# Kernel tuning notes

Measured on AMD Instinct MI355X. Metric: run time of the kernel, lower is better.

The kernel has to match this reference:

```python
import jax, jax.numpy as jnp
import numpy as np

V = 50000
E = 300000
B = 4
LAT = 512
H = 128
L = 3


def setup_inputs() -> dict:
    key = jax.random.key(0)
    ks = jax.random.split(key, 8)
    vertex_xyz = jax.random.normal(ks[0], (V, 3), jnp.float32)
    latent = jax.random.normal(ks[1], (B, LAT), jnp.float32)
    edge_index = jax.random.randint(ks[2], (2, E), 0, V, dtype=jnp.int32)
    def lin(k, out_f, in_f):
        return jax.random.normal(k, (out_f, in_f), jnp.float32) / np.float32(np.sqrt(in_f))
    W_in = lin(ks[3], H, LAT + 3)
    b_in = jnp.zeros((H,), jnp.float32)
    conv_W = jax.random.normal(ks[4], (L, H, H), jnp.float32) / np.float32(np.sqrt(H))
    conv_b = jnp.zeros((L, H), jnp.float32)
    W_out = lin(ks[5], 3, H)
    b_out = jnp.zeros((3,), jnp.float32)
    return dict(vertex_xyz=vertex_xyz, latent=latent, edge_index=edge_index,
                W_in=W_in, b_in=b_in, conv_W=conv_W, conv_b=conv_b,
                W_out=W_out, b_out=b_out)


def _edge_norm(edge_index, B_, V_):
    """GCN symmetric normalization for edge_index tiled B times (same node ids,
    as in the original code's edge_index.repeat(1, B)) plus self-loops on all
    N = B*V flattened nodes. Structure is identical across layers, so compute once."""
    N = B_ * V_
    ei = jnp.tile(edge_index, (1, B_))                 # (2, E*B), ids in [0, V)
    loops = jnp.arange(N, dtype=edge_index.dtype)
    row = jnp.concatenate([ei[0], loops])              # source
    col = jnp.concatenate([ei[1], loops])              # target
    deg = jax.ops.segment_sum(jnp.ones(row.shape, jnp.float32), col, num_segments=N)
    dis = jnp.where(deg > 0, jax.lax.rsqrt(jnp.maximum(deg, 1.0)), 0.0)
    norm = dis[row] * dis[col]                         # (E*B + N,)
    return row, col, norm, N


def reference(vertex_xyz, latent, edge_index, W_in, b_in, conv_W, conv_b, W_out, b_out):
    B_, V_ = latent.shape[0], vertex_xyz.shape[0]
    row, col, norm, N = _edge_norm(edge_index, B_, V_)

    # concat template xyz with broadcast latent -> (B*V, LAT+3)
    x = jnp.concatenate([
        jnp.broadcast_to(vertex_xyz[None], (B_, V_, 3)),
        jnp.broadcast_to(latent[:, None, :], (B_, V_, latent.shape[-1])),
    ], axis=-1).reshape(B_ * V_, -1)

    x = jax.nn.relu(x @ W_in.T + b_in)                 # (N, H)

    for l in range(conv_W.shape[0]):
        h = x @ conv_W[l].T                            # linear (no bias before aggregation)
        agg = jax.ops.segment_sum(norm[:, None] * h[row], col, num_segments=N)
        x = jax.nn.relu(agg + conv_b[l])

    out = x @ W_out.T + b_out                          # (N, 3)
    return out.reshape(B_, V_, 3)
```

## Files before the change

kernel.cpp:

```cpp
#include <hip/hip_runtime.h>
#include <hip/hip_bf16.h>

typedef __attribute__((ext_vector_type(8))) short short8;
typedef __attribute__((ext_vector_type(4))) float f32x4;

#define V_ 50000
#define E_ 300000
#define B_ 4
#define LAT_ 512
#define H_ 128
#define L_ 3
#define N_ (B_*V_)

#define SCAN_B 512
#define SCAN_G ((V_ + SCAN_B - 1) / SCAN_B)

__device__ inline void bsplit(float v, ushort& hi, ushort& lo) {
    __hip_bfloat16 hb = __float2bfloat16(v);
    float hf = __bfloat162float(hb);
    __hip_bfloat16 lb = __float2bfloat16(v - hf);
    hi = *(ushort*)&hb; lo = *(ushort*)&lb;
}
__device__ inline float bjoin(ushort h, ushort l) {
    __hip_bfloat16 hb = *(__hip_bfloat16*)&h;
    __hip_bfloat16 lb = *(__hip_bfloat16*)&l;
    return __bfloat162float(hb) + __bfloat162float(lb);
}
__device__ inline int swzr(int row) { return ((row & 7) << 4) ^ ((row & 8) << 2); }


__global__ void k_zero(int* __restrict__ deg, int* __restrict__ cursor) {
    int i = blockIdx.x * 256 + threadIdx.x;
    if (i < V_) { deg[i] = 0; cursor[i] = 0; }
}

__global__ void k_deg(const int* __restrict__ dst, int* __restrict__ deg) {
    int e = blockIdx.x * 256 + threadIdx.x;
    if (e < E_) atomicAdd(&deg[dst[e]], 1);
}

__global__ __launch_bounds__(SCAN_B) void k_scan1(const int* __restrict__ deg,
                                                  int* __restrict__ off,
                                                  float* __restrict__ dis,
                                                  int* __restrict__ part) {
    int t = threadIdx.x;
    int i = blockIdx.x * SCAN_B + t;
    int d = (i < V_) ? deg[i] : 0;
    __shared__ int sm[SCAN_B];
    sm[t] = d;
    __syncthreads();
    int val = d;
    for (int s = 1; s < SCAN_B; s <<= 1) {
        int o = (t >= s) ? sm[t - s] : 0;
        __syncthreads();
        val += o;
        sm[t] = val;
        __syncthreads();
    }
    if (i < V_) {
        off[i] = val - d;
        dis[i] = rsqrtf((float)(B_ * d + 1));
    }
    if (t == SCAN_B - 1) part[blockIdx.x] = val;
}

__global__ void k_scan2(int* __restrict__ part) {
    __shared__ int sm[128];
    int t = threadIdx.x;
    int v = (t < SCAN_G) ? part[t] : 0;
    sm[t] = v;
    __syncthreads();
    int val = v;
    for (int s = 1; s < 128; s <<= 1) {
        int o = (t >= s) ? sm[t - s] : 0;
        __syncthreads();
        val += o;
        sm[t] = val;
        __syncthreads();
    }
    if (t < SCAN_G) part[t] = val - v;
}

__global__ __launch_bounds__(SCAN_B) void k_scan3(int* __restrict__ off,
                                                  const int* __restrict__ part) {
    int i = blockIdx.x * SCAN_B + threadIdx.x;
    if (i < V_) off[i] += part[blockIdx.x];
    if (i == 0) off[V_] = E_;
}

__global__ void k_fill(const int* __restrict__ src, const int* __restrict__ dst,
                       const int* __restrict__ off, int* __restrict__ cursor,
                       int* __restrict__ csr) {
    int e = blockIdx.x * 256 + threadIdx.x;
    if (e < E_) {
        int c = dst[e];
        int p = atomicAdd(&cursor[c], 1);
        csr[off[c] + p] = src[e];
    }
}


__global__ void k_wsplit(const float* __restrict__ W, ushort* __restrict__ Whi,
                         ushort* __restrict__ Wlo) {
    int i = blockIdx.x * 256 + threadIdx.x;
    float w = W[i];
    ushort hi, lo; bsplit(w, hi, lo);
    Whi[i] = hi; Wlo[i] = lo;
}

__global__ void k_prep(const float* __restrict__ Win, float* __restrict__ Wxyz) {
    int j = threadIdx.x;
    f32x4 v = {Win[(size_t)j*(LAT_+3)+0], Win[(size_t)j*(LAT_+3)+1],
               Win[(size_t)j*(LAT_+3)+2], 0.f};
    *(f32x4*)(Wxyz + j*4) = v;
}

__global__ void k_latproj(const float* __restrict__ Win, const float* __restrict__ bin,
                          const float* __restrict__ latent, float* __restrict__ latproj) {
    int t = blockIdx.x * 128 + threadIdx.x;
    if (t >= B_ * H_) return;
    int b = t >> 7, j = t & 127;
    const float* wr = Win + (size_t)j * (LAT_ + 3) + 3;
    const float* lp = latent + (size_t)b * LAT_;
    float s = bin[j];
    for (int k = 0; k < LAT_; k++) s = fmaf(wr[k], lp[k], s);
    latproj[t] = s;
}


__global__ __launch_bounds__(512, 2) void k_big(
        const float* __restrict__ xyz, const float* __restrict__ latproj,
        const float* __restrict__ Wxyz,
        const ushort* __restrict__ Whi, const ushort* __restrict__ Wlo,
        const float* __restrict__ convb,
        const float* __restrict__ Wout, const float* __restrict__ bout,
        float* __restrict__ out) {
    __shared__ __align__(16) char smem[32768];
    const int tid = threadIdx.x;
    const int row0 = V_ + blockIdx.x * 64;
    const int lane = tid & 63;
    const int wid  = tid >> 6;
    const int l15  = lane & 15;
    const int kg   = lane >> 4;
    const int n0   = wid * 16;
    const int tr   = tid >> 4;
    const int c0   = (tid & 15) * 8;

#pragma unroll
    for (int rep = 0; rep < 2; rep++) {
        int row = tr + rep * 32;
        int node = row0 + row;
        ushort hs[8], ls[8];
        if (node < N_) {
            int v = node % V_, b = node / V_;
            float xv0 = xyz[v*3+0], xv1 = xyz[v*3+1], xv2 = xyz[v*3+2];
#pragma unroll
            for (int i = 0; i < 8; i++) {
                int j = c0 + i;
                f32x4 wx = *(const f32x4*)(Wxyz + j*4);
                float s = latproj[b*H_ + j];
                s = fmaf(wx[0], xv0, s);
                s = fmaf(wx[1], xv1, s);
                s = fmaf(wx[2], xv2, s);
                s = fmaxf(s, 0.f);
                bsplit(s, hs[i], ls[i]);
            }
        } else {
#pragma unroll
            for (int i = 0; i < 8; i++) { hs[i] = 0; ls[i] = 0; }
        }
        int bo = (c0*2) ^ swzr(row);
        *(uint4*)(smem + row*256 + bo) = *(uint4*)hs;
        *(uint4*)(smem + 16384 + row*256 + bo) = *(uint4*)ls;
    }
    __syncthreads();

    for (int l = 0; l < L_; l++) {
        const ushort* Whp = Whi + (size_t)l*H_*H_;
        const ushort* Wlp = Wlo + (size_t)l*H_*H_;
        short8 wh[4], wl[4];
#pragma unroll
        for (int ks = 0; ks < 4; ks++) {
            const ushort* bh = Whp + (size_t)(n0 + l15)*H_ + ks*32 + kg*4;
            const ushort* bl = Wlp + (size_t)(n0 + l15)*H_ + ks*32 + kg*4;
            union { short8 v; uint2 u[2]; } uh, ul;
            uh.u[0] = *(const uint2*)bh;  uh.u[1] = *(const uint2*)(bh + 16);
            ul.u[0] = *(const uint2*)bl;  ul.u[1] = *(const uint2*)(bl + 16);
            wh[ks] = uh.v; wl[ks] = ul.v;
        }
        f32x4 acc[4];
#pragma unroll
        for (int mt = 0; mt < 4; mt++) acc[mt] = (f32x4){0.f,0.f,0.f,0.f};
#pragma unroll
        for (int mt = 0; mt < 4; mt++) {
            int row = mt*16 + l15;
            int sw = swzr(row);
            const char* rbh = smem + row*256;
            const char* rbl = smem + 16384 + row*256;
#pragma unroll
            for (int ks = 0; ks < 4; ks++) {
                int cc = ks*64 + kg*8;
                union { short8 v; uint2 u[2]; } ah, al;
                ah.u[0] = *(const uint2*)(rbh + (cc ^ sw));
                ah.u[1] = *(const uint2*)(rbh + ((cc+32) ^ sw));
                al.u[0] = *(const uint2*)(rbl + (cc ^ sw));
                al.u[1] = *(const uint2*)(rbl + ((cc+32) ^ sw));
                acc[mt] = __builtin_amdgcn_mfma_f32_16x16x32_bf16(ah.v, wh[ks], acc[mt], 0,0,0);
                acc[mt] = __builtin_amdgcn_mfma_f32_16x16x32_bf16(al.v, wh[ks], acc[mt], 0,0,0);
                acc[mt] = __builtin_amdgcn_mfma_f32_16x16x32_bf16(ah.v, wl[ks], acc[mt], 0,0,0);
            }
        }
        __syncthreads();
        float bv = convb[l*H_ + n0 + l15];
        int bo = (n0 + l15) * 2;
#pragma unroll
        for (int mt = 0; mt < 4; mt++)
#pragma unroll
            for (int j = 0; j < 4; j++) {
                int row = mt*16 + kg*4 + j;
                int sw = swzr(row);
                float v = fmaxf(acc[mt][j] + bv, 0.f);
                ushort hi, lo; bsplit(v, hi, lo);
                *(ushort*)(smem + row*256 + (bo ^ sw)) = hi;
                *(ushort*)(smem + 16384 + row*256 + (bo ^ sw)) = lo;
            }
        __syncthreads();
    }

    float wo0[8], wo1[8], wo2[8];
#pragma unroll
    for (int i = 0; i < 8; i++) {
        wo0[i] = Wout[0*H_ + c0 + i];
        wo1[i] = Wout[1*H_ + c0 + i];
        wo2[i] = Wout[2*H_ + c0 + i];
    }
#pragma unroll
    for (int rep = 0; rep < 2; rep++) {
        int row = tr + rep*32;
        int node = row0 + row;
        int bo = (c0*2) ^ swzr(row);
        uint4 uh = *(const uint4*)(smem + row*256 + bo);
        uint4 ul = *(const uint4*)(smem + 16384 + row*256 + bo);
        const ushort* hp = (const ushort*)&uh;
        const ushort* lp = (const ushort*)&ul;
        float p0 = 0.f, p1 = 0.f, p2 = 0.f;
#pragma unroll
        for (int i = 0; i < 8; i++) {
            float xv = bjoin(hp[i], lp[i]);
            p0 = fmaf(xv, wo0[i], p0);
            p1 = fmaf(xv, wo1[i], p1);
            p2 = fmaf(xv, wo2[i], p2);
        }
#pragma unroll
        for (int m = 1; m < 16; m <<= 1) {
            p0 += __shfl_xor(p0, m);
            p1 += __shfl_xor(p1, m);
            p2 += __shfl_xor(p2, m);
        }
        if ((tid & 15) == 0 && node < N_) {
            out[(size_t)node*3 + 0] = p0 + bout[0];
            out[(size_t)node*3 + 1] = p1 + bout[1];
            out[(size_t)node*3 + 2] = p2 + bout[2];
        }
    }
}


template<int MODE>
__global__ __launch_bounds__(512, 2) void k_lay0(
        const ushort* __restrict__ xh, const ushort* __restrict__ xl,
        const float* __restrict__ xyz, const float* __restrict__ latproj,
        const float* __restrict__ Wxyz,
        const ushort* __restrict__ Whp, const ushort* __restrict__ Wlp,
        float* __restrict__ h) {
    __shared__ __align__(16) char smem[32768];
    const int tid = threadIdx.x;
    const int row0 = blockIdx.x * 64;
    const int lane = tid & 63;
    const int wid  = tid >> 6;
    const int l15  = lane & 15;
    const int kg   = lane >> 4;
    const int n0   = wid * 16;
    const int tr   = tid >> 4;
    const int c0   = (tid & 15) * 8;

    if (MODE == 0) {
#pragma unroll
        for (int rep = 0; rep < 2; rep++) {
            int row = tr + rep * 32;
            int v = row0 + row;
            ushort hs[8], ls[8];
            if (v < V_) {
                float xv0 = xyz[v*3+0], xv1 = xyz[v*3+1], xv2 = xyz[v*3+2];
#pragma unroll
                for (int i = 0; i < 8; i++) {
                    int j = c0 + i;
                    f32x4 wx = *(const f32x4*)(Wxyz + j*4);
                    float s = latproj[j];
                    s = fmaf(wx[0], xv0, s);
                    s = fmaf(wx[1], xv1, s);
                    s = fmaf(wx[2], xv2, s);
                    s = fmaxf(s, 0.f);
                    bsplit(s, hs[i], ls[i]);
                }
            } else {
#pragma unroll
                for (int i = 0; i < 8; i++) { hs[i] = 0; ls[i] = 0; }
            }
            int bo = (c0*2) ^ swzr(row);
            *(uint4*)(smem + row*256 + bo) = *(uint4*)hs;
            *(uint4*)(smem + 16384 + row*256 + bo) = *(uint4*)ls;
        }
    } else {
#pragma unroll
        for (int k = 0; k < 4; k++) {
            int chunk = tid + k*512;
            int p  = chunk >> 10;
            int r  = (chunk >> 4) & 63;
            int cb = (chunk & 15) * 16;
            int grow = row0 + r;
            uint4 g = {0u,0u,0u,0u};
            if (grow < V_)
                g = *(const uint4*)((const char*)((p ? xl : xh) + (size_t)grow*H_) + cb);
            *(uint4*)(smem + p*16384 + r*256 + (cb ^ swzr(r))) = g;
        }
    }
    __syncthreads();

    short8 wh[4], wl[4];
#pragma unroll
    for (int ks = 0; ks < 4; ks++) {
        const ushort* bh = Whp + (size_t)(n0 + l15)*H_ + ks*32 + kg*4;
        const ushort* bl = Wlp + (size_t)(n0 + l15)*H_ + ks*32 + kg*4;
        union { short8 v; uint2 u[2]; } uh, ul;
        uh.u[0] = *(const uint2*)bh;  uh.u[1] = *(const uint2*)(bh + 16);
        ul.u[0] = *(const uint2*)bl;  ul.u[1] = *(const uint2*)(bl + 16);
        wh[ks] = uh.v; wl[ks] = ul.v;
    }

    f32x4 acc[4];
#pragma unroll
    for (int mt = 0; mt < 4; mt++) acc[mt] = (f32x4){0.f,0.f,0.f,0.f};
#pragma unroll
    for (int mt = 0; mt < 4; mt++) {
        int row = mt*16 + l15;
        int sw = swzr(row);
        const char* rbh = smem + row*256;
        const char* rbl = smem + 16384 + row*256;
#pragma unroll
        for (int ks = 0; ks < 4; ks++) {
            int cc = ks*64 + kg*8;
            union { short8 v; uint2 u[2]; } ah, al;
            ah.u[0] = *(const uint2*)(rbh + (cc ^ sw));
            ah.u[1] = *(const uint2*)(rbh + ((cc+32) ^ sw));
            al.u[0] = *(const uint2*)(rbl + (cc ^ sw));
            al.u[1] = *(const uint2*)(rbl + ((cc+32) ^ sw));
            acc[mt] = __builtin_amdgcn_mfma_f32_16x16x32_bf16(ah.v, wh[ks], acc[mt], 0,0,0);
            acc[mt] = __builtin_amdgcn_mfma_f32_16x16x32_bf16(al.v, wh[ks], acc[mt], 0,0,0);
            acc[mt] = __builtin_amdgcn_mfma_f32_16x16x32_bf16(ah.v, wl[ks], acc[mt], 0,0,0);
        }
    }

#pragma unroll
    for (int mt = 0; mt < 4; mt++)
#pragma unroll
        for (int j = 0; j < 4; j++) {
            int grow = row0 + mt*16 + kg*4 + j;
            if (grow < V_) h[(size_t)grow*H_ + n0 + l15] = acc[mt][j];
        }
}


template<bool FINAL>
__global__ __launch_bounds__(256) void k_agg0(const float* __restrict__ h,
                                              const float* __restrict__ dis,
                                              const int* __restrict__ off,
                                              const int* __restrict__ csr,
                                              const float* __restrict__ bias,
                                              ushort* __restrict__ xh_out,
                                              ushort* __restrict__ xl_out,
                                              const float* __restrict__ Wout,
                                              const float* __restrict__ bout,
                                              float* __restrict__ out) {
    int c = blockIdx.x * 4 + (threadIdx.x >> 6);
    int lane = threadIdx.x & 63;
    if (c >= V_) return;
    int beg = off[c], end = off[c + 1];
    int nu = end - beg;
    int   myu  = (lane < nu) ? csr[beg + lane] : 0;
    float mywu = (lane < nu) ? dis[myu] : 0.f;
    float a0 = 0.f, a1 = 0.f;
    int nn = nu < 64 ? nu : 64;
    for (int i = 0; i < nn; i++) {
        int u = __shfl(myu, i);
        float wu = __shfl(mywu, i);
        const float* hu = h + (size_t)u * 128;
        a0 = fmaf(wu, hu[lane],      a0);
        a1 = fmaf(wu, hu[lane + 64], a1);
    }
    for (int i = beg + 64; i < end; i++) {
        int u = csr[i];
        float wu = dis[u];
        const float* hu = h + (size_t)u * 128;
        a0 = fmaf(wu, hu[lane],      a0);
        a1 = fmaf(wu, hu[lane + 64], a1);
    }
    float dc = dis[c];
    const float* hr = h + (size_t)c * 128;
    float s0 = fmaxf(dc * (float)B_ * a0 + dc * dc * hr[lane]      + bias[lane],      0.f);
    float s1 = fmaxf(dc * (float)B_ * a1 + dc * dc * hr[lane + 64] + bias[lane + 64], 0.f);
    if (FINAL) {
        float p0 = s0 * Wout[0*H_ + lane] + s1 * Wout[0*H_ + 64 + lane];
        float p1 = s0 * Wout[1*H_ + lane] + s1 * Wout[1*H_ + 64 + lane];
        float p2 = s0 * Wout[2*H_ + lane] + s1 * Wout[2*H_ + 64 + lane];
#pragma unroll
        for (int d = 32; d; d >>= 1) {
            p0 += __shfl_down(p0, d);
            p1 += __shfl_down(p1, d);
            p2 += __shfl_down(p2, d);
        }
        if (lane == 0) {
            out[(size_t)c*3 + 0] = p0 + bout[0];
            out[(size_t)c*3 + 1] = p1 + bout[1];
            out[(size_t)c*3 + 2] = p2 + bout[2];
        }
    } else {
        ushort h0, l0, h1, l1;
        bsplit(s0, h0, l0);
        bsplit(s1, h1, l1);
        xh_out[(size_t)c*128 + lane]      = h0;
        xl_out[(size_t)c*128 + lane]      = l0;
        xh_out[(size_t)c*128 + lane + 64] = h1;
        xl_out[(size_t)c*128 + lane + 64] = l1;
    }
}


extern "C" void kernel_launch(void* const* d_in, const int* in_sizes, int n_in,
                              void* d_out, int out_size, void* d_ws, size_t ws_size,
                              hipStream_t stream) {
    const float* xyz    = (const float*)d_in[0];
    const float* latent = (const float*)d_in[1];
    const int*   ei     = (const int*)d_in[2];
    const float* Win    = (const float*)d_in[3];
    const float* bin    = (const float*)d_in[4];
    const float* convW  = (const float*)d_in[5];
    const float* convb  = (const float*)d_in[6];
    const float* Wout   = (const float*)d_in[7];
    const float* bout   = (const float*)d_in[8];
    float* out = (float*)d_out;

    char* w = (char*)d_ws;
    auto carve = [&](size_t bytes) {
        char* p = w;
        w += (bytes + 255) & ~(size_t)255;
        return p;
    };
    ushort* xh      = (ushort*)carve((size_t)V_ * H_ * 2);
    ushort* xl      = (ushort*)carve((size_t)V_ * H_ * 2);
    float*  h       = (float*)carve((size_t)V_ * H_ * 4);
    ushort* Whi     = (ushort*)carve((size_t)L_ * H_ * H_ * 2);
    ushort* Wlo     = (ushort*)carve((size_t)L_ * H_ * H_ * 2);
    float*  dis     = (float*)carve((size_t)V_ * 4);
    float*  latproj = (float*)carve((size_t)B_ * H_ * 4);
    float*  Wxyz    = (float*)carve((size_t)H_ * 4 * 4);
    int*    deg     = (int*)carve((size_t)V_ * 4);
    int*    off     = (int*)carve((size_t)(V_ + 1) * 4);
    int*    cursor  = (int*)carve((size_t)V_ * 4);
    int*    csr     = (int*)carve((size_t)E_ * 4);
    int*    part    = (int*)carve((size_t)SCAN_G * 4);
    (void)ws_size; (void)in_sizes; (void)n_in; (void)out_size;

    const int* src = ei;
    const int* dst = ei + E_;

    k_zero<<<(V_ + 255) / 256, 256, 0, stream>>>(deg, cursor);
    k_deg<<<(E_ + 255) / 256, 256, 0, stream>>>(dst, deg);
    k_scan1<<<SCAN_G, SCAN_B, 0, stream>>>(deg, off, dis, part);
    k_scan2<<<1, 128, 0, stream>>>(part);
    k_scan3<<<SCAN_G, SCAN_B, 0, stream>>>(off, part);
    k_fill<<<(E_ + 255) / 256, 256, 0, stream>>>(src, dst, off, cursor, csr);

    k_wsplit<<<(L_ * H_ * H_) / 256, 256, 0, stream>>>(convW, Whi, Wlo);
    k_prep<<<1, 128, 0, stream>>>(Win, Wxyz);
    k_latproj<<<4, 128, 0, stream>>>(Win, bin, latent, latproj);

    k_big<<<(N_ - V_ + 63) / 64, 512, 0, stream>>>(xyz, latproj, Wxyz, Whi, Wlo,
                                                   convb, Wout, bout, out);

    const int GB0 = (V_ + 63) / 64;
    k_lay0<0><<<GB0, 512, 0, stream>>>(nullptr, nullptr, xyz, latproj, Wxyz,
                                       Whi, Wlo, h);
    k_agg0<false><<<(V_ + 3) / 4, 256, 0, stream>>>(h, dis, off, csr, convb,
                                                    xh, xl, nullptr, nullptr, nullptr);
    k_lay0<1><<<GB0, 512, 0, stream>>>(xh, xl, nullptr, nullptr, nullptr,
                                       Whi + (size_t)1*H_*H_, Wlo + (size_t)1*H_*H_, h);
    k_agg0<false><<<(V_ + 3) / 4, 256, 0, stream>>>(h, dis, off, csr, convb + 1*H_,
                                                    xh, xl, nullptr, nullptr, nullptr);
    k_lay0<1><<<GB0, 512, 0, stream>>>(xh, xl, nullptr, nullptr, nullptr,
                                       Whi + (size_t)2*H_*H_, Wlo + (size_t)2*H_*H_, h);
    k_agg0<true><<<(V_ + 3) / 4, 256, 0, stream>>>(h, dis, off, csr, convb + 2*H_,
                                                   nullptr, nullptr, Wout, bout, out);
}
```

Baseline: 416.1 us.

## Keep GEMM activations in registers, stream weights as A-operand, drop LDS round-trips

Restructures the dense MLP kernels so each wave owns 32 nodes and holds their activations as MFMA B-fragments in registers. Weight tiles are streamed as the A operand, and layer outputs are converted straight back into B-fragments without going through shared memory or block barriers. This removes the LDS staging, the swizzled stores and the __syncthreads between layers in k_big and k_lay0, and lets k_lay0 write vectorised f32x4 outputs. In exchange every wave reloads all of W from global/L2 for each layer, and register pressure rises with the 16 accumulators plus fragments.

```diff
diff --git a/kernel.cpp b/kernel.cpp
--- a/kernel.cpp
+++ b/kernel.cpp
@@ -21,12 +21,6 @@
     __hip_bfloat16 lb = __float2bfloat16(v - hf);
     hi = *(ushort*)&hb; lo = *(ushort*)&lb;
 }
-__device__ inline float bjoin(ushort h, ushort l) {
-    __hip_bfloat16 hb = *(__hip_bfloat16*)&h;
-    __hip_bfloat16 lb = *(__hip_bfloat16*)&l;
-    return __bfloat162float(hb) + __bfloat162float(lb);
-}
-__device__ inline int swzr(int row) { return ((row & 7) << 4) ^ ((row & 8) << 2); }
 
 
 __global__ void k_zero(int* __restrict__ deg, int* __restrict__ cursor) {
@@ -128,246 +122,219 @@
 }
 
 
-__global__ __launch_bounds__(512, 2) void k_big(
+__device__ inline void gemm_layer(const ushort* __restrict__ Ah,
+                                  const ushort* __restrict__ Al,
+                                  int l15, int kg,
+                                  const short8 bh[4][2], const short8 bl[4][2],
+                                  f32x4 acc[8][2]) {
+#pragma unroll
+    for (int m = 0; m < 8; m++) {
+        const ushort* ph = Ah + (m*16 + l15)*H_ + kg*4;
+        const ushort* pl = Al + (m*16 + l15)*H_ + kg*4;
+        short8 ah[4], al[4];
+#pragma unroll
+        for (int ks = 0; ks < 4; ks++) {
+            union { short8 v; uint2 u[2]; } uh, ul;
+            uh.u[0] = *(const uint2*)(ph + ks*32);
+            uh.u[1] = *(const uint2*)(ph + ks*32 + 16);
+            ul.u[0] = *(const uint2*)(pl + ks*32);
+            ul.u[1] = *(const uint2*)(pl + ks*32 + 16);
+            ah[ks] = uh.v; al[ks] = ul.v;
+        }
+#pragma unroll
+        for (int ks = 0; ks < 4; ks++)
+#pragma unroll
+            for (int nt = 0; nt < 2; nt++) {
+                acc[m][nt] = __builtin_amdgcn_mfma_f32_16x16x32_bf16(ah[ks], bh[ks][nt], acc[m][nt], 0,0,0);
+                acc[m][nt] = __builtin_amdgcn_mfma_f32_16x16x32_bf16(ah[ks], bl[ks][nt], acc[m][nt], 0,0,0);
+                acc[m][nt] = __builtin_amdgcn_mfma_f32_16x16x32_bf16(al[ks], bh[ks][nt], acc[m][nt], 0,0,0);
+            }
+    }
+}
+
+__device__ inline void acc_to_bfrag(const f32x4 acc[8][2], const float* __restrict__ bias,
+                                    int kg, short8 bh[4][2], short8 bl[4][2]) {
+#pragma unroll
+    for (int t = 0; t < 4; t++)
+#pragma unroll
+        for (int nt = 0; nt < 2; nt++) {
+            union { short8 v; ushort s[8]; } uh, ul;
+#pragma unroll
+            for (int q = 0; q < 2; q++) {
+                int m = 2*t + q;
+                f32x4 b4 = *(const f32x4*)(bias + m*16 + kg*4);
+#pragma unroll
+                for (int j = 0; j < 4; j++) {
+                    float s = fmaxf(acc[m][nt][j] + b4[j], 0.f);
+                    bsplit(s, uh.s[q*4+j], ul.s[q*4+j]);
+                }
+            }
+            bh[t][nt] = uh.v; bl[t][nt] = ul.v;
+        }
+}
+
+__device__ inline void x0_bfrag(const float* __restrict__ xyz, const float* __restrict__ lp,
+                                const float* __restrict__ Wxyz, int v, bool ok, int kg, int nt,
+                                short8 bh[4][2], short8 bl[4][2]) {
+    float x0 = xyz[v*3+0], x1 = xyz[v*3+1], x2 = xyz[v*3+2];
+#pragma unroll
+    for (int ks = 0; ks < 4; ks++) {
+        union { short8 v; ushort s[8]; } uh, ul;
+#pragma unroll
+        for (int q = 0; q < 2; q++)
+#pragma unroll
+            for (int j = 0; j < 4; j++) {
+                int f = ks*32 + q*16 + kg*4 + j;
+                f32x4 wx = *(const f32x4*)(Wxyz + f*4);
+                float s = lp[f];
+                s = fmaf(wx[0], x0, s);
+                s = fmaf(wx[1], x1, s);
+                s = fmaf(wx[2], x2, s);
+                s = fmaxf(s, 0.f);
+                if (!ok) s = 0.f;
+                bsplit(s, uh.s[q*4+j], ul.s[q*4+j]);
+            }
+        bh[ks][nt] = uh.v; bl[ks][nt] = ul.v;
+    }
+}
+
+
+__global__ __launch_bounds__(256, 2) void k_big2(
         const float* __restrict__ xyz, const float* __restrict__ latproj,
         const float* __restrict__ Wxyz,
         const ushort* __restrict__ Whi, const ushort* __restrict__ Wlo,
         const float* __restrict__ convb,
         const float* __restrict__ Wout, const float* __restrict__ bout,
         float* __restrict__ out) {
-    __shared__ __align__(16) char smem[32768];
-    const int tid = threadIdx.x;
-    const int row0 = V_ + blockIdx.x * 64;
+    const int tid  = threadIdx.x;
     const int lane = tid & 63;
-    const int wid  = tid >> 6;
     const int l15  = lane & 15;
     const int kg   = lane >> 4;
-    const int n0   = wid * 16;
-    const int tr   = tid >> 4;
-    const int c0   = (tid & 15) * 8;
-
-#pragma unroll
-    for (int rep = 0; rep < 2; rep++) {
-        int row = tr + rep * 32;
-        int node = row0 + row;
-        ushort hs[8], ls[8];
-        if (node < N_) {
-            int v = node % V_, b = node / V_;
-            float xv0 = xyz[v*3+0], xv1 = xyz[v*3+1], xv2 = xyz[v*3+2];
-#pragma unroll
-            for (int i = 0; i < 8; i++) {
-                int j = c0 + i;
-                f32x4 wx = *(const f32x4*)(Wxyz + j*4);
-                float s = latproj[b*H_ + j];
-                s = fmaf(wx[0], xv0, s);
-                s = fmaf(wx[1], xv1, s);
-                s = fmaf(wx[2], xv2, s);
-                s = fmaxf(s, 0.f);
-                bsplit(s, hs[i], ls[i]);
-            }
-        } else {
-#pragma unroll
-            for (int i = 0; i < 8; i++) { hs[i] = 0; ls[i] = 0; }
-        }
-        int bo = (c0*2) ^ swzr(row);
-        *(uint4*)(smem + row*256 + bo) = *(uint4*)hs;
-        *(uint4*)(smem + 16384 + row*256 + bo) = *(uint4*)ls;
-    }
-    __syncthreads();
-
+    const int base = V_ + (blockIdx.x * 4 + (tid >> 6)) * 32;
+
+    int node[2], vv[2]; bool ok[2];
+    const float* lp[2];
+#pragma unroll
+    for (int nt = 0; nt < 2; nt++) {
+        int n = base + nt*16 + l15;
+        ok[nt] = (n < N_);
+        int nn = ok[nt] ? n : 0;
+        node[nt] = nn;
+        int b = nn / V_;
+        vv[nt] = nn - b * V_;
+        lp[nt] = latproj + b * H_;
+    }
+
+    short8 bh[4][2], bl[4][2];
+#pragma unroll
+    for (int nt = 0; nt < 2; nt++)
+        x0_bfrag(xyz, lp[nt], Wxyz, vv[nt], ok[nt], kg, nt, bh, bl);
+
+    f32x4 acc[8][2];
     for (int l = 0; l < L_; l++) {
-        const ushort* Whp = Whi + (size_t)l*H_*H_;
-        const ushort* Wlp = Wlo + (size_t)l*H_*H_;
-        short8 wh[4], wl[4];
-#pragma unroll
-        for (int ks = 0; ks < 4; ks++) {
-            const ushort* bh = Whp + (size_t)(n0 + l15)*H_ + ks*32 + kg*4;
-            const ushort* bl = Wlp + (size_t)(n0 + l15)*H_ + ks*32 + kg*4;
-            union { short8 v; uint2 u[2]; } uh, ul;
-            uh.u[0] = *(const uint2*)bh;  uh.u[1] = *(const uint2*)(bh + 16);
-            ul.u[0] = *(const uint2*)bl;  ul.u[1] = *(const uint2*)(bl + 16);
-            wh[ks] = uh.v; wl[ks] = ul.v;
-        }
-        f32x4 acc[4];
-#pragma unroll
-        for (int mt = 0; mt < 4; mt++) acc[mt] = (f32x4){0.f,0.f,0.f,0.f};
-#pragma unroll
-        for (int mt = 0; mt < 4; mt++) {
-            int row = mt*16 + l15;
-            int sw = swzr(row);
-            const char* rbh = smem + row*256;
-            const char* rbl = smem + 16384 + row*256;
-#pragma unroll
-            for (int ks = 0; ks < 4; ks++) {
-                int cc = ks*64 + kg*8;
-                union { short8 v; uint2 u[2]; } ah, al;
-                ah.u[0] = *(const uint2*)(rbh + (cc ^ sw));
-                ah.u[1] = *(const uint2*)(rbh + ((cc+32) ^ sw));
-                al.u[0] = *(const uint2*)(rbl + (cc ^ sw));
-                al.u[1] = *(const uint2*)(rbl + ((cc+32) ^ sw));
-                acc[mt] = __builtin_amdgcn_mfma_f32_16x16x32_bf16(ah.v, wh[ks], acc[mt], 0,0,0);
-                acc[mt] = __builtin_amdgcn_mfma_f32_16x16x32_bf16(al.v, wh[ks], acc[mt], 0,0,0);
-                acc[mt] = __builtin_amdgcn_mfma_f32_16x16x32_bf16(ah.v, wl[ks], acc[mt], 0,0,0);
-            }
-        }
-        __syncthreads();
-        float bv = convb[l*H_ + n0 + l15];
-        int bo = (n0 + l15) * 2;
-#pragma unroll
-        for (int mt = 0; mt < 4; mt++)
+#pragma unroll
+        for (int m = 0; m < 8; m++)
+#pragma unroll
+            for (int nt = 0; nt < 2; nt++) acc[m][nt] = (f32x4){0.f,0.f,0.f,0.f};
+        gemm_layer(Whi + (size_t)l*H_*H_, Wlo + (size_t)l*H_*H_, l15, kg, bh, bl, acc);
+        if (l < L_ - 1)
+            acc_to_bfrag(acc, convb + l*H_, kg, bh, bl);
+    }
+
+    float p[2][3];
+#pragma unroll
+    for (int nt = 0; nt < 2; nt++) { p[nt][0] = 0.f; p[nt][1] = 0.f; p[nt][2] = 0.f; }
+#pragma unroll
+    for (int m = 0; m < 8; m++) {
+        f32x4 b4 = *(const f32x4*)(convb + 2*H_ + m*16 + kg*4);
+        f32x4 w0 = *(const f32x4*)(Wout + 0*H_ + m*16 + kg*4);
+        f32x4 w1 = *(const f32x4*)(Wout + 1*H_ + m*16 + kg*4);
+        f32x4 w2 = *(const f32x4*)(Wout + 2*H_ + m*16 + kg*4);
+#pragma unroll
+        for (int nt = 0; nt < 2; nt++)
 #pragma unroll
             for (int j = 0; j < 4; j++) {
-                int row = mt*16 + kg*4 + j;
-                int sw = swzr(row);
-                float v = fmaxf(acc[mt][j] + bv, 0.f);
-                ushort hi, lo; bsplit(v, hi, lo);
-                *(ushort*)(smem + row*256 + (bo ^ sw)) = hi;
-                *(ushort*)(smem + 16384 + row*256 + (bo ^ sw)) = lo;
-            }
-        __syncthreads();
-    }
-
-    float wo0[8], wo1[8], wo2[8];
-#pragma unroll
-    for (int i = 0; i < 8; i++) {
-        wo0[i] = Wout[0*H_ + c0 + i];
-        wo1[i] = Wout[1*H_ + c0 + i];
-        wo2[i] = Wout[2*H_ + c0 + i];
-    }
-#pragma unroll
-    for (int rep = 0; rep < 2; rep++) {
-        int row = tr + rep*32;
-        int node = row0 + row;
-        int bo = (c0*2) ^ swzr(row);
-        uint4 uh = *(const uint4*)(smem + row*256 + bo);
-        uint4 ul = *(const uint4*)(smem + 16384 + row*256 + bo);
-        const ushort* hp = (const ushort*)&uh;
-        const ushort* lp = (const ushort*)&ul;
-        float p0 = 0.f, p1 = 0.f, p2 = 0.f;
-#pragma unroll
-        for (int i = 0; i < 8; i++) {
-            float xv = bjoin(hp[i], lp[i]);
-            p0 = fmaf(xv, wo0[i], p0);
-            p1 = fmaf(xv, wo1[i], p1);
-            p2 = fmaf(xv, wo2[i], p2);
-        }
-#pragma unroll
-        for (int m = 1; m < 16; m <<= 1) {
-            p0 += __shfl_xor(p0, m);
-            p1 += __shfl_xor(p1, m);
-            p2 += __shfl_xor(p2, m);
-        }
-        if ((tid & 15) == 0 && node < N_) {
-            out[(size_t)node*3 + 0] = p0 + bout[0];
-            out[(size_t)node*3 + 1] = p1 + bout[1];
-            out[(size_t)node*3 + 2] = p2 + bout[2];
-        }
+                float s = fmaxf(acc[m][nt][j] + b4[j], 0.f);
+                p[nt][0] = fmaf(s, w0[j], p[nt][0]);
+                p[nt][1] = fmaf(s, w1[j], p[nt][1]);
+                p[nt][2] = fmaf(s, w2[j], p[nt][2]);
+            }
+    }
+#pragma unroll
+    for (int nt = 0; nt < 2; nt++)
+#pragma unroll
+        for (int o = 0; o < 3; o++) {
+            p[nt][o] += __shfl_xor(p[nt][o], 16);
+            p[nt][o] += __shfl_xor(p[nt][o], 32);
+        }
+    if (kg == 0) {
+#pragma unroll
+        for (int nt = 0; nt < 2; nt++)
+            if (ok[nt]) {
+                out[(size_t)node[nt]*3 + 0] = p[nt][0] + bout[0];
+                out[(size_t)node[nt]*3 + 1] = p[nt][1] + bout[1];
+                out[(size_t)node[nt]*3 + 2] = p[nt][2] + bout[2];
+            }
     }
 }
 
 
 template<int MODE>
-__global__ __launch_bounds__(512, 2) void k_lay0(
+__global__ __launch_bounds__(256, 2) void k_lay0(
         const ushort* __restrict__ xh, const ushort* __restrict__ xl,
         const float* __restrict__ xyz, const float* __restrict__ latproj,
         const float* __restrict__ Wxyz,
         const ushort* __restrict__ Whp, const ushort* __restrict__ Wlp,
         float* __restrict__ h) {
-    __shared__ __align__(16) char smem[32768];
-    const int tid = threadIdx.x;
-    const int row0 = blockIdx.x * 64;
+    const int tid  = threadIdx.x;
     const int lane = tid & 63;
-    const int wid  = tid >> 6;
     const int l15  = lane & 15;
     const int kg   = lane >> 4;
-    const int n0   = wid * 16;
-    const int tr   = tid >> 4;
-    const int c0   = (tid & 15) * 8;
-
+    const int base = (blockIdx.x * 4 + (tid >> 6)) * 32;
+
+    int node[2]; bool ok[2];
+#pragma unroll
+    for (int nt = 0; nt < 2; nt++) {
+        int n = base + nt*16 + l15;
+        ok[nt] = (n < V_);
+        node[nt] = ok[nt] ? n : 0;
+    }
+
+    short8 bh[4][2], bl[4][2];
     if (MODE == 0) {
 #pragma unroll
-        for (int rep = 0; rep < 2; rep++) {
-            int row = tr + rep * 32;
-            int v = row0 + row;
-            ushort hs[8], ls[8];
-            if (v < V_) {
-                float xv0 = xyz[v*3+0], xv1 = xyz[v*3+1], xv2 = xyz[v*3+2];
-#pragma unroll
-                for (int i = 0; i < 8; i++) {
-                    int j = c0 + i;
-                    f32x4 wx = *(const f32x4*)(Wxyz + j*4);
-                    float s = latproj[j];
-                    s = fmaf(wx[0], xv0, s);
-                    s = fmaf(wx[1], xv1, s);
-                    s = fmaf(wx[2], xv2, s);
-                    s = fmaxf(s, 0.f);
-                    bsplit(s, hs[i], ls[i]);
-                }
-            } else {
-#pragma unroll
-                for (int i = 0; i < 8; i++) { hs[i] = 0; ls[i] = 0; }
-            }
-            int bo = (c0*2) ^ swzr(row);
-            *(uint4*)(smem + row*256 + bo) = *(uint4*)hs;
-            *(uint4*)(smem + 16384 + row*256 + bo) = *(uint4*)ls;
-        }
+        for (int nt = 0; nt < 2; nt++)
+            x0_bfrag(xyz, latproj, Wxyz, node[nt], ok[nt], kg, nt, bh, bl);
     } else {
 #pragma unroll
-        for (int k = 0; k < 4; k++) {
-            int chunk = tid + k*512;
-            int p  = chunk >> 10;
-            int r  = (chunk >> 4) & 63;
-            int cb = (chunk & 15) * 16;
-            int grow = row0 + r;
-            uint4 g = {0u,0u,0u,0u};
-            if (grow < V_)
-                g = *(const uint4*)((const char*)((p ? xl : xh) + (size_t)grow*H_) + cb);
-            *(uint4*)(smem + p*16384 + r*256 + (cb ^ swzr(r))) = g;
-        }
-    }
-    __syncthreads();
-
-    short8 wh[4], wl[4];
-#pragma unroll
-    for (int ks = 0; ks < 4; ks++) {
-        const ushort* bh = Whp + (size_t)(n0 + l15)*H_ + ks*32 + kg*4;
-        const ushort* bl = Wlp + (size_t)(n0 + l15)*H_ + ks*32 + kg*4;
-        union { short8 v; uint2 u[2]; } uh, ul;
-        uh.u[0] = *(const uint2*)bh;  uh.u[1] = *(const uint2*)(bh + 16);
-        ul.u[0] = *(const uint2*)bl;  ul.u[1] = *(const uint2*)(bl + 16);
-        wh[ks] = uh.v; wl[ks] = ul.v;
-    }
-
-    f32x4 acc[4];
-#pragma unroll
-    for (int mt = 0; mt < 4; mt++) acc[mt] = (f32x4){0.f,0.f,0.f,0.f};
-#pragma unroll
-    for (int mt = 0; mt < 4; mt++) {
-        int row = mt*16 + l15;
-        int sw = swzr(row);
-        const char* rbh = smem + row*256;
-        const char* rbl = smem + 16384 + row*256;
-#pragma unroll
-        for (int ks = 0; ks < 4; ks++) {
-            int cc = ks*64 + kg*8;
-            union { short8 v; uint2 u[2]; } ah, al;
-            ah.u[0] = *(const uint2*)(rbh + (cc ^ sw));
-            ah.u[1] = *(const uint2*)(rbh + ((cc+32) ^ sw));
-            al.u[0] = *(const uint2*)(rbl + (cc ^ sw));
-            al.u[1] = *(const uint2*)(rbl + ((cc+32) ^ sw));
-            acc[mt] = __builtin_amdgcn_mfma_f32_16x16x32_bf16(ah.v, wh[ks], acc[mt], 0,0,0);
-            acc[mt] = __builtin_amdgcn_mfma_f32_16x16x32_bf16(al.v, wh[ks], acc[mt], 0,0,0);
-            acc[mt] = __builtin_amdgcn_mfma_f32_16x16x32_bf16(ah.v, wl[ks], acc[mt], 0,0,0);
-        }
-    }
-
-#pragma unroll
-    for (int mt = 0; mt < 4; mt++)
-#pragma unroll
-        for (int j = 0; j < 4; j++) {
-            int grow = row0 + mt*16 + kg*4 + j;
-            if (grow < V_) h[(size_t)grow*H_ + n0 + l15] = acc[mt][j];
-        }
+        for (int nt = 0; nt < 2; nt++) {
+            const ushort* ph = xh + (size_t)node[nt]*H_ + kg*4;
+            const ushort* pl = xl + (size_t)node[nt]*H_ + kg*4;
+#pragma unroll
+            for (int ks = 0; ks < 4; ks++) {
+                union { short8 v; uint2 u[2]; } uh, ul;
+                uh.u[0] = *(const uint2*)(ph + ks*32);
+                uh.u[1] = *(const uint2*)(ph + ks*32 + 16);
+                ul.u[0] = *(const uint2*)(pl + ks*32);
+                ul.u[1] = *(const uint2*)(pl + ks*32 + 16);
+                bh[ks][nt] = uh.v; bl[ks][nt] = ul.v;
+            }
+        }
+    }
+
+    f32x4 acc[8][2];
+#pragma unroll
+    for (int m = 0; m < 8; m++)
+#pragma unroll
+        for (int nt = 0; nt < 2; nt++) acc[m][nt] = (f32x4){0.f,0.f,0.f,0.f};
+    gemm_layer(Whp, Wlp, l15, kg, bh, bl, acc);
+
+#pragma unroll
+    for (int m = 0; m < 8; m++)
+#pragma unroll
+        for (int nt = 0; nt < 2; nt++)
+            if (ok[nt])
+                *(f32x4*)(h + (size_t)node[nt]*H_ + m*16 + kg*4) = acc[m][nt];
 }
 
 
@@ -485,20 +452,21 @@
     k_prep<<<1, 128, 0, stream>>>(Win, Wxyz);
     k_latproj<<<4, 128, 0, stream>>>(Win, bin, latent, latproj);
 
-    k_big<<<(N_ - V_ + 63) / 64, 512, 0, stream>>>(xyz, latproj, Wxyz, Whi, Wlo,
-                                                   convb, Wout, bout, out);
-
-    const int GB0 = (V_ + 63) / 64;
-    k_lay0<0><<<GB0, 512, 0, stream>>>(nullptr, nullptr, xyz, latproj, Wxyz,
-                                       Whi, Wlo, h);
+    const int GB = ((N_ - V_) + 127) / 128;
+    k_big2<<<GB, 256, 0, stream>>>(xyz, latproj, Wxyz, Whi, Wlo,
+                                   convb, Wout, bout, out);
+
+    const int G0 = (V_ + 127) / 128;
+    k_lay0<0><<<G0, 256, 0, stream>>>(nullptr, nullptr, xyz, latproj, Wxyz,
+                                      Whi, Wlo, h);
     k_agg0<false><<<(V_ + 3) / 4, 256, 0, stream>>>(h, dis, off, csr, convb,
                                                     xh, xl, nullptr, nullptr, nullptr);
-    k_lay0<1><<<GB0, 512, 0, stream>>>(xh, xl, nullptr, nullptr, nullptr,
-                                       Whi + (size_t)1*H_*H_, Wlo + (size_t)1*H_*H_, h);
+    k_lay0<1><<<G0, 256, 0, stream>>>(xh, xl, nullptr, nullptr, nullptr,
+                                      Whi + (size_t)1*H_*H_, Wlo + (size_t)1*H_*H_, h);
     k_agg0<false><<<(V_ + 3) / 4, 256, 0, stream>>>(h, dis, off, csr, convb + 1*H_,
                                                     xh, xl, nullptr, nullptr, nullptr);
-    k_lay0<1><<<GB0, 512, 0, stream>>>(xh, xl, nullptr, nullptr, nullptr,
-                                       Whi + (size_t)2*H_*H_, Wlo + (size_t)2*H_*H_, h);
+    k_lay0<1><<<G0, 256, 0, stream>>>(xh, xl, nullptr, nullptr, nullptr,
+                                      Whi + (size_t)2*H_*H_, Wlo + (size_t)2*H_*H_, h);
     k_agg0<true><<<(V_ + 3) / 4, 256, 0, stream>>>(h, dis, off, csr, convb + 2*H_,
                                                    nullptr, nullptr, Wout, bout, out);
 }
```

Result: slower. 511.4 us (+22.9%).
